# Optimization experiments

Measured on AMD Instinct MI355X. Metric: run time of the kernel, lower is better.

## Reference

```python
import jax, jax.numpy as jnp
import numpy as np

B, L, D = 2, 2048, 1024
H, HD = 16, 64
MAX_LEN = 4096


def rotate_half(t):
    t1, t2 = jnp.split(t, 2, axis=-1)
    return jnp.concatenate([-t2, t1], axis=-1)


def setup_inputs() -> dict:
    key = jax.random.key(0)
    ks = jax.random.split(key, 6)
    # rope tables computed the standard way (cos/sin of position*inv_freq)
    inv_freq = 1.0 / (10000.0 ** (np.arange(0, HD, 2, dtype=np.float32) / HD))
    pos = np.arange(MAX_LEN, dtype=np.float32)
    freqs = np.einsum('l,f->lf', pos, inv_freq)          # [MAX_LEN, HD/2]
    emb = np.concatenate([freqs, freqs], axis=-1)        # [MAX_LEN, HD]
    return {
        'x': jax.random.normal(ks[0], (B, L, D), dtype=jnp.float32),
        'rope_cos': jnp.asarray(np.cos(emb)),
        'rope_sin': jnp.asarray(np.sin(emb)),
        'W_qkv': jax.random.normal(ks[1], (D, 3 * H * HD), dtype=jnp.float32) * (D ** -0.5),
        'W_out': jax.random.normal(ks[2], (H * HD, D), dtype=jnp.float32) * ((H * HD) ** -0.5),
        'b_out': jnp.zeros((D,), dtype=jnp.float32),
    }


def reference(x, rope_cos, rope_sin, W_qkv, W_out, b_out):
    Bb, Ll, Dd = x.shape
    qkv = jnp.einsum('bld,de->ble', x, W_qkv)            # fused QKV projection
    q, k, v = jnp.split(qkv, 3, axis=-1)
    # [B, h, L, d]
    q = q.reshape(Bb, Ll, H, HD).transpose(0, 2, 1, 3)
    k = k.reshape(Bb, Ll, H, HD).transpose(0, 2, 1, 3)
    v = v.reshape(Bb, Ll, H, HD).transpose(0, 2, 1, 3)
    cos = rope_cos[:Ll][None, None, :, :]                # [1,1,L,d]
    sin = rope_sin[:Ll][None, None, :, :]
    q = q * cos + rotate_half(q) * sin
    k = k * cos + rotate_half(k) * sin
    # causal scaled dot-product attention
    scale = HD ** -0.5
    scores = jnp.einsum('bhqd,bhkd->bhqk', q, k) * scale
    causal = jnp.tril(jnp.ones((Ll, Ll), dtype=bool))
    scores = jnp.where(causal[None, None], scores, jnp.finfo(scores.dtype).min)
    attn = jax.nn.softmax(scores, axis=-1)
    out = jnp.einsum('bhqk,bhkd->bhqd', attn, v)
    out = out.transpose(0, 2, 1, 3).reshape(Bb, Ll, H * HD)
    return jnp.einsum('ble,ed->bld', out, W_out) + b_out
```

## Files before the change

kernel.cpp:

```cpp
#include <hip/hip_runtime.h>
#include <math.h>

#define BQ 2
#define LQ 2048
#define DQ 1024
#define HQ 16
#define HDQ 64

typedef __bf16 bf16_t;
typedef bf16_t bf16x4 __attribute__((ext_vector_type(4)));
typedef bf16_t bf16x8 __attribute__((ext_vector_type(8)));
typedef _Float16 f16_t;
typedef f16_t f16x4 __attribute__((ext_vector_type(4)));
typedef f16_t f16x8 __attribute__((ext_vector_type(8)));
typedef float f32x4 __attribute__((ext_vector_type(4)));

__global__ __launch_bounds__(256) void prep_kernel(
    const float* __restrict__ x, const float* __restrict__ Wqkv,
    const float* __restrict__ Wout, const float* __restrict__ cosT,
    const float* __restrict__ sinT,
    bf16_t* __restrict__ xb, bf16_t* __restrict__ Wqkvt,
    bf16_t* __restrict__ Wot, float4* __restrict__ rpk)
{
    __shared__ float t[32][33];
    const int bid = blockIdx.x, tid = threadIdx.x;
    if (bid < 4096) {
        const int i = (bid * 256 + tid) * 4;
        float4 v = *(const float4*)(x + i);
        bf16x4 o;
        o[0] = (bf16_t)v.x; o[1] = (bf16_t)v.y; o[2] = (bf16_t)v.z; o[3] = (bf16_t)v.w;
        *(bf16x4*)(xb + i) = o;
    } else if (bid < 8192) {
        const bool isq = bid < 7168;
        const int b = isq ? bid - 4096 : bid - 7168;
        const int N = isq ? 3072 : 1024;
        const int gx = isq ? 96 : 32;
        const float* in = isq ? Wqkv : Wout;
        bf16_t* out = isq ? Wqkvt : Wot;
        const int k0 = (b / gx) * 32, n0 = (b % gx) * 32;
        const int r = tid >> 3, c4 = (tid & 7) * 4;
        float4 v = *(const float4*)(in + (size_t)(k0 + r) * N + n0 + c4);
        t[r][c4 + 0] = v.x; t[r][c4 + 1] = v.y;
        t[r][c4 + 2] = v.z; t[r][c4 + 3] = v.w;
        __syncthreads();
        bf16x4 o;
        o[0] = (bf16_t)t[c4 + 0][r]; o[1] = (bf16_t)t[c4 + 1][r];
        o[2] = (bf16_t)t[c4 + 2][r]; o[3] = (bf16_t)t[c4 + 3][r];
        *(bf16x4*)(out + (size_t)(n0 + r) * 1024 + k0 + c4) = o;
    } else {
        const int idx = (bid - 8192) * 256 + tid;
        const int i = idx & 15, l = idx >> 4;
        rpk[idx] = make_float4(cosT[l * 64 + i], cosT[l * 64 + 16 + i],
                               sinT[l * 64 + i], sinT[l * 64 + 16 + i]);
    }
}

__global__ __launch_bounds__(256) void qkv_gemm_kernel(
    const bf16_t* __restrict__ A, const bf16_t* __restrict__ Bt,
    bf16_t* __restrict__ qo, bf16_t* __restrict__ ko, f16_t* __restrict__ vo,
    const float4* __restrict__ rpk)
{
    __shared__ __align__(16) bf16_t As[128][64];
    __shared__ __align__(16) bf16_t Bs[128][64];
    const int K = 1024;
    const int tid  = threadIdx.x;
    const int lane = tid & 63;
    const int w    = tid >> 6;
    const int lr   = lane & 15, quad = lane >> 4;
    const int wm   = w & 1, wn = w >> 1;
    const int m0   = blockIdx.y * 128, n0 = blockIdx.x * 128;
    const int srow8 = lane >> 3;
    const int swz   = ((lane & 7) ^ srow8) * 8;
    const int wc    = (lane & 7) * 8;

    f32x4 acc[4][4];
#pragma unroll
    for (int i = 0; i < 4; i++)
#pragma unroll
        for (int j = 0; j < 4; j++)
#pragma unroll
            for (int r = 0; r < 4; r++) acc[i][j][r] = 0.f;

    bf16x8 ar[4], br[4];
#pragma unroll
    for (int j = 0; j < 4; j++) {
        const int rr = (w * 4 + j) * 8 + srow8;
        ar[j] = *(const bf16x8*)(A  + (size_t)(m0 + rr) * K + swz);
        br[j] = *(const bf16x8*)(Bt + (size_t)(n0 + rr) * K + swz);
    }

    for (int k0 = 0; k0 < K; k0 += 64) {
        __syncthreads();
#pragma unroll
        for (int j = 0; j < 4; j++) {
            const int rg = (w * 4 + j) * 8 + srow8;
            *(bf16x8*)(&As[rg][wc]) = ar[j];
            *(bf16x8*)(&Bs[rg][wc]) = br[j];
        }
        __syncthreads();
        if (k0 + 64 < K) {
#pragma unroll
            for (int j = 0; j < 4; j++) {
                const int rr = (w * 4 + j) * 8 + srow8;
                ar[j] = *(const bf16x8*)(A  + (size_t)(m0 + rr) * K + k0 + 64 + swz);
                br[j] = *(const bf16x8*)(Bt + (size_t)(n0 + rr) * K + k0 + 64 + swz);
            }
        }

        bf16x8 af[4][2], bfr[4][2];
#pragma unroll
        for (int t = 0; t < 4; t++)
#pragma unroll
            for (int h = 0; h < 2; h++) {
                const int cA = ((quad + 4 * h) ^ (lr & 7)) * 8;
                af[t][h]  = *(const bf16x8*)(&As[wm * 64 + t * 16 + lr][cA]);
                bfr[t][h] = *(const bf16x8*)(&Bs[wn * 64 + t * 16 + lr][cA]);
            }
#pragma unroll
        for (int h = 0; h < 2; h++)
#pragma unroll
            for (int mt = 0; mt < 4; mt++)
#pragma unroll
                for (int nt = 0; nt < 4; nt++)
                    acc[mt][nt] = __builtin_amdgcn_mfma_f32_16x16x32_bf16(
                        af[mt][h], bfr[nt][h], acc[mt][nt], 0, 0, 0);
    }

    const int which = n0 >> 10;
    const int h = ((n0 & 1023) + wn * 64) >> 6;
    if (which == 2) {
#pragma unroll
        for (int mt = 0; mt < 4; mt++) {
            const int m = m0 + wm * 64 + mt * 16 + quad * 4;
            const int b = m >> 11, l = m & 2047;
            f16_t* p = vo + ((size_t)(b * HQ + h) * HDQ) * LQ + l;
#pragma unroll
            for (int nt = 0; nt < 4; nt++) {
                f16x4 pv;
#pragma unroll
                for (int r = 0; r < 4; r++) pv[r] = (f16_t)acc[mt][nt][r];
                *(f16x4*)(p + (size_t)(nt * 16 + lr) * LQ) = pv;
            }
        }
    } else {
        bf16_t* dst = which ? ko : qo;
        const float qs = which ? 1.0f : 0.18033688011f;
#pragma unroll
        for (int mt = 0; mt < 4; mt++)
#pragma unroll
            for (int r = 0; r < 4; r++) {
                const int m = m0 + wm * 64 + mt * 16 + quad * 4 + r;
                const int b = m >> 11, l = m & 2047;
                const float4 rp = rpk[l * 16 + lr];
                const float a0 = acc[mt][0][r], a1 = acc[mt][1][r];
                const float a2 = acc[mt][2][r], a3 = acc[mt][3][r];
                bf16_t* p = dst + ((size_t)(b * HQ + h) * LQ + l) * HDQ;
                p[lr]      = (bf16_t)((a0 * rp.x - a2 * rp.z) * qs);
                p[16 + lr] = (bf16_t)((a1 * rp.y - a3 * rp.w) * qs);
                p[32 + lr] = (bf16_t)((a2 * rp.x + a0 * rp.z) * qs);
                p[48 + lr] = (bf16_t)((a3 * rp.y + a1 * rp.w) * qs);
            }
    }
}

__global__ __launch_bounds__(256) void out_gemm_kernel(
    const bf16_t* __restrict__ A, const bf16_t* __restrict__ Bt,
    float* __restrict__ fo, const float* __restrict__ bias)
{
    __shared__ __align__(16) bf16_t As[64][64];
    __shared__ __align__(16) bf16_t Bs[128][64];
    const int K = 1024, N = 1024;
    const int tid  = threadIdx.x;
    const int lane = tid & 63;
    const int w    = tid >> 6;
    const int lr   = lane & 15, quad = lane >> 4;
    const int m0   = blockIdx.y * 64, n0 = blockIdx.x * 128;
    const int srow8 = lane >> 3;
    const int swz   = ((lane & 7) ^ srow8) * 8;
    const int wc    = (lane & 7) * 8;

    f32x4 acc[4][2];
#pragma unroll
    for (int i = 0; i < 4; i++)
#pragma unroll
        for (int j = 0; j < 2; j++)
#pragma unroll
            for (int r = 0; r < 4; r++) acc[i][j][r] = 0.f;

    bf16x8 ar[2], br[4];
#pragma unroll
    for (int j = 0; j < 2; j++)
        ar[j] = *(const bf16x8*)(A + (size_t)(m0 + (w * 2 + j) * 8 + srow8) * K + swz);
#pragma unroll
    for (int j = 0; j < 4; j++)
        br[j] = *(const bf16x8*)(Bt + (size_t)(n0 + (w * 4 + j) * 8 + srow8) * K + swz);

    for (int k0 = 0; k0 < K; k0 += 64) {
        __syncthreads();
#pragma unroll
        for (int j = 0; j < 2; j++)
            *(bf16x8*)(&As[(w * 2 + j) * 8 + srow8][wc]) = ar[j];
#pragma unroll
        for (int j = 0; j < 4; j++)
            *(bf16x8*)(&Bs[(w * 4 + j) * 8 + srow8][wc]) = br[j];
        __syncthreads();
        if (k0 + 64 < K) {
#pragma unroll
            for (int j = 0; j < 2; j++)
                ar[j] = *(const bf16x8*)(A + (size_t)(m0 + (w * 2 + j) * 8 + srow8) * K
                                          + k0 + 64 + swz);
#pragma unroll
            for (int j = 0; j < 4; j++)
                br[j] = *(const bf16x8*)(Bt + (size_t)(n0 + (w * 4 + j) * 8 + srow8) * K
                                          + k0 + 64 + swz);
        }

        bf16x8 af[4][2], bfr[2][2];
#pragma unroll
        for (int h = 0; h < 2; h++) {
            const int cA = ((quad + 4 * h) ^ (lr & 7)) * 8;
#pragma unroll
            for (int t = 0; t < 4; t++)
                af[t][h] = *(const bf16x8*)(&As[t * 16 + lr][cA]);
#pragma unroll
            for (int t = 0; t < 2; t++)
                bfr[t][h] = *(const bf16x8*)(&Bs[w * 32 + t * 16 + lr][cA]);
        }
#pragma unroll
        for (int h = 0; h < 2; h++)
#pragma unroll
            for (int mt = 0; mt < 4; mt++)
#pragma unroll
                for (int nt = 0; nt < 2; nt++)
                    acc[mt][nt] = __builtin_amdgcn_mfma_f32_16x16x32_bf16(
                        af[mt][h], bfr[nt][h], acc[mt][nt], 0, 0, 0);
    }

#pragma unroll
    for (int nt = 0; nt < 2; nt++) {
        const int n = n0 + w * 32 + nt * 16 + lr;
        const float bj = bias[n];
#pragma unroll
        for (int mt = 0; mt < 4; mt++)
#pragma unroll
            for (int r = 0; r < 4; r++) {
                const int m = m0 + mt * 16 + quad * 4 + r;
                fo[(size_t)m * N + n] = acc[mt][nt][r] + bj;
            }
    }
}

__global__ __launch_bounds__(512) void attn_kernel10(
    const bf16_t* __restrict__ qb, const bf16_t* __restrict__ kb,
    const f16_t* __restrict__ vtb, bf16_t* __restrict__ ob)
{
    __shared__ __align__(16) bf16_t Kb[2][64][64];
    __shared__ __align__(16) f16_t  Vs[2][64][68];

    const int tid  = threadIdx.x;
    const int lane = tid & 63;
    const int w    = tid >> 6;
    const int quad = lane >> 4;
    const int lr   = lane & 15;
    const int bh   = blockIdx.x;
    const int qt2  = 15 - blockIdx.y;

    const bf16_t* Kh = kb  + (size_t)bh * LQ * HDQ;
    const f16_t*  Vh = vtb + (size_t)bh * HDQ * LQ;

    const int r0  = tid >> 3;
    const int c0  = (tid & 7) * 8;
    const int ksw = ((tid & 7) ^ (r0 & 7)) * 8;

    f16x4 ones;
#pragma unroll
    for (int j = 0; j < 4; j++) ones[j] = (f16_t)1.0f;

    const int qbase = qt2 * 128 + w * 16;
    const int qrow  = qbase + lr;
    const bf16_t* qp = qb + ((size_t)bh * LQ + qrow) * HDQ;
    const bf16x8 qa0 = *(const bf16x8*)(qp + quad * 8);
    const bf16x8 qa1 = *(const bf16x8*)(qp + 32 + quad * 8);

    const int nkt = 2 * qt2 + 2;

    bf16x8 kp = *(const bf16x8*)(Kh + (size_t)r0 * HDQ + c0);
    f16x8  vp = *(const f16x8*)(Vh + (size_t)r0 * LQ + c0);

    f32x4 Oacc[4], lacc;
#pragma unroll
    for (int d = 0; d < 4; d++)
#pragma unroll
        for (int r = 0; r < 4; r++) Oacc[d][r] = 0.f;
#pragma unroll
    for (int r = 0; r < 4; r++) lacc[r] = 0.f;

    for (int kt = 0; kt < nkt; kt++) {
        const int buf = kt & 1;
        *(bf16x8*)(&Kb[buf][r0][ksw]) = kp;
        *(f16x8*)(&Vs[buf][r0][c0]) = vp;
        __syncthreads();
        if (kt + 1 < nkt) {
            kp = *(const bf16x8*)(Kh + (size_t)((kt + 1) * 64 + r0) * HDQ + c0);
            vp = *(const f16x8*)(Vh + (size_t)r0 * LQ + (kt + 1) * 64 + c0);
        }

        if (kt * 64 <= qbase + 15) {
            f32x4 s[4];
            __builtin_amdgcn_s_setprio(1);
#pragma unroll
            for (int nt = 0; nt < 4; nt++) {
                const int rsw = lr & 7;
                const bf16x8 kf0 = *(const bf16x8*)(&Kb[buf][nt * 16 + lr][(quad ^ rsw) * 8]);
                const bf16x8 kf1 = *(const bf16x8*)(&Kb[buf][nt * 16 + lr][((quad + 4) ^ rsw) * 8]);
                f32x4 z = {0.f, 0.f, 0.f, 0.f};
                z = __builtin_amdgcn_mfma_f32_16x16x32_bf16(kf0, qa0, z, 0, 0, 0);
                z = __builtin_amdgcn_mfma_f32_16x16x32_bf16(kf1, qa1, z, 0, 0, 0);
                s[nt] = z;
            }
            __builtin_amdgcn_s_setprio(0);
            if (kt * 64 + 63 > qbase) {
#pragma unroll
                for (int nt = 0; nt < 4; nt++)
#pragma unroll
                    for (int r = 0; r < 4; r++)
                        if (kt * 64 + nt * 16 + quad * 4 + r > qrow) s[nt][r] = -INFINITY;
            }
            f16x4 pa[4];
#pragma unroll
            for (int nt = 0; nt < 4; nt++)
#pragma unroll
                for (int r = 0; r < 4; r++)
                    pa[nt][r] = (f16_t)__builtin_amdgcn_exp2f(s[nt][r]);

            __builtin_amdgcn_s_setprio(1);
#pragma unroll
            for (int d = 0; d < 4; d++)
#pragma unroll
                for (int nt = 0; nt < 4; nt++) {
                    const f16x4 vf = *(const f16x4*)(&Vs[buf][d * 16 + lr][nt * 16 + quad * 4]);
                    Oacc[d] = __builtin_amdgcn_mfma_f32_16x16x16f16(pa[nt], vf, Oacc[d], 0, 0, 0);
                }
#pragma unroll
            for (int nt = 0; nt < 4; nt++)
                lacc = __builtin_amdgcn_mfma_f32_16x16x16f16(pa[nt], ones, lacc, 0, 0, 0);
            __builtin_amdgcn_s_setprio(0);
        }
    }

    const int b = bh >> 4, h = bh & 15;
#pragma unroll
    for (int r = 0; r < 4; r++) {
        const float inv = 1.0f / lacc[r];
        const int q = qbase + quad * 4 + r;
        bf16_t* op = ob + ((size_t)(b * LQ + q)) * 1024 + h * 64;
#pragma unroll
        for (int d = 0; d < 4; d++)
            op[d * 16 + lr] = (bf16_t)(Oacc[d][r] * inv);
    }
}

extern "C" void kernel_launch(void* const* d_in, const int* in_sizes, int n_in,
                              void* d_out, int out_size, void* d_ws, size_t ws_size,
                              hipStream_t stream) {
    const float* x        = (const float*)d_in[0];
    const float* rope_cos = (const float*)d_in[1];
    const float* rope_sin = (const float*)d_in[2];
    const float* W_qkv    = (const float*)d_in[3];
    const float* W_out    = (const float*)d_in[4];
    const float* b_out    = (const float*)d_in[5];
    float* out = (float*)d_out;

    char* wsb = (char*)d_ws;
    bf16_t* xb    = (bf16_t*)(wsb);
    bf16_t* qbf   = (bf16_t*)(wsb + ((size_t)8  << 20));
    bf16_t* kbf   = (bf16_t*)(wsb + ((size_t)16 << 20));
    f16_t*  vth   = (f16_t*) (wsb + ((size_t)24 << 20));
    bf16_t* ob    = (bf16_t*)(wsb + ((size_t)32 << 20));
    bf16_t* Wqkvt = (bf16_t*)(wsb + ((size_t)40 << 20));
    bf16_t* Wot   = (bf16_t*)(wsb + ((size_t)46 << 20));
    float4* rpk   = (float4*)(wsb + ((size_t)48 << 20));

    prep_kernel<<<8320, 256, 0, stream>>>(x, W_qkv, W_out, rope_cos, rope_sin,
                                          xb, Wqkvt, Wot, rpk);

    dim3 g1(3072 / 128, 4096 / 128);
    qkv_gemm_kernel<<<g1, 256, 0, stream>>>(xb, Wqkvt, qbf, kbf, vth, rpk);

    dim3 g2(32, 16);
    attn_kernel10<<<g2, 512, 0, stream>>>(qbf, kbf, vth, ob);

    dim3 g3(1024 / 128, 4096 / 64);
    out_gemm_kernel<<<g3, 256, 0, stream>>>(ob, Wot, out, b_out);
}
```

Baseline: 172.3 us.

## Double-buffer QKV GEMM shared tiles with K=32 stages and two-deep register prefetch

Restructures the QKV projection GEMM main loop from single-buffered 64-wide K tiles to double-buffered 32-wide K tiles in LDS, with two register stages of global prefetch. Each iteration now has one barrier instead of two, so writes to one LDS buffer can overlap MFMA work on the other. The LDS swizzle is changed to match the narrower tiles. The trade-off is more loop iterations with fewer MFMAs per barrier, plus extra registers for the second prefetch stage.

```diff
diff --git a/kernel.cpp b/kernel.cpp
--- a/kernel.cpp
+++ b/kernel.cpp
@@ -60,8 +60,8 @@
     bf16_t* __restrict__ qo, bf16_t* __restrict__ ko, f16_t* __restrict__ vo,
     const float4* __restrict__ rpk)
 {
-    __shared__ __align__(16) bf16_t As[128][64];
-    __shared__ __align__(16) bf16_t Bs[128][64];
+    __shared__ __align__(16) bf16_t As[2][128][32];
+    __shared__ __align__(16) bf16_t Bs[2][128][32];
     const int K = 1024;
     const int tid  = threadIdx.x;
     const int lane = tid & 63;
@@ -69,9 +69,16 @@
     const int lr   = lane & 15, quad = lane >> 4;
     const int wm   = w & 1, wn = w >> 1;
     const int m0   = blockIdx.y * 128, n0 = blockIdx.x * 128;
-    const int srow8 = lane >> 3;
-    const int swz   = ((lane & 7) ^ srow8) * 8;
-    const int wc    = (lane & 7) * 8;
+
+    const int sr  = tid >> 2;
+    const int sc  = tid & 3;
+    const int sw  = (sc ^ ((sr >> 1) & 3)) * 8;
+    const int rdc = (quad ^ ((lr >> 1) & 3)) * 8;
+
+    const bf16_t* Ar0 = A  + (size_t)(m0 + sr) * K + sc * 8;
+    const bf16_t* Ar1 = A  + (size_t)(m0 + sr + 64) * K + sc * 8;
+    const bf16_t* Br0 = Bt + (size_t)(n0 + sr) * K + sc * 8;
+    const bf16_t* Br1 = Bt + (size_t)(n0 + sr + 64) * K + sc * 8;
 
     f32x4 acc[4][4];
 #pragma unroll
@@ -81,50 +88,53 @@
 #pragma unroll
             for (int r = 0; r < 4; r++) acc[i][j][r] = 0.f;
 
-    bf16x8 ar[4], br[4];
-#pragma unroll
-    for (int j = 0; j < 4; j++) {
-        const int rr = (w * 4 + j) * 8 + srow8;
-        ar[j] = *(const bf16x8*)(A  + (size_t)(m0 + rr) * K + swz);
-        br[j] = *(const bf16x8*)(Bt + (size_t)(n0 + rr) * K + swz);
-    }
-
-    for (int k0 = 0; k0 < K; k0 += 64) {
-        __syncthreads();
-#pragma unroll
-        for (int j = 0; j < 4; j++) {
-            const int rg = (w * 4 + j) * 8 + srow8;
-            *(bf16x8*)(&As[rg][wc]) = ar[j];
-            *(bf16x8*)(&Bs[rg][wc]) = br[j];
-        }
-        __syncthreads();
-        if (k0 + 64 < K) {
-#pragma unroll
-            for (int j = 0; j < 4; j++) {
-                const int rr = (w * 4 + j) * 8 + srow8;
-                ar[j] = *(const bf16x8*)(A  + (size_t)(m0 + rr) * K + k0 + 64 + swz);
-                br[j] = *(const bf16x8*)(Bt + (size_t)(n0 + rr) * K + k0 + 64 + swz);
-            }
-        }
-
-        bf16x8 af[4][2], bfr[4][2];
-#pragma unroll
-        for (int t = 0; t < 4; t++)
-#pragma unroll
-            for (int h = 0; h < 2; h++) {
-                const int cA = ((quad + 4 * h) ^ (lr & 7)) * 8;
-                af[t][h]  = *(const bf16x8*)(&As[wm * 64 + t * 16 + lr][cA]);
-                bfr[t][h] = *(const bf16x8*)(&Bs[wn * 64 + t * 16 + lr][cA]);
-            }
-#pragma unroll
-        for (int h = 0; h < 2; h++)
-#pragma unroll
-            for (int mt = 0; mt < 4; mt++)
-#pragma unroll
-                for (int nt = 0; nt < 4; nt++)
-                    acc[mt][nt] = __builtin_amdgcn_mfma_f32_16x16x32_bf16(
-                        af[mt][h], bfr[nt][h], acc[mt][nt], 0, 0, 0);
-    }
+#define QLOAD(A0, A1, B0, B1, t) do {                      \
+        A0 = *(const bf16x8*)(Ar0 + (t) * 32);             \
+        A1 = *(const bf16x8*)(Ar1 + (t) * 32);             \
+        B0 = *(const bf16x8*)(Br0 + (t) * 32);             \
+        B1 = *(const bf16x8*)(Br1 + (t) * 32);             \
+    } while (0)
+#define QWRITE(A0, A1, B0, B1, bf) do {                    \
+        *(bf16x8*)(&As[bf][sr][sw])      = A0;             \
+        *(bf16x8*)(&As[bf][sr + 64][sw]) = A1;             \
+        *(bf16x8*)(&Bs[bf][sr][sw])      = B0;             \
+        *(bf16x8*)(&Bs[bf][sr + 64][sw]) = B1;             \
+    } while (0)
+#define QCOMP(bf) do {                                                        \
+        bf16x8 af[4], bfr[4];                                                 \
+        _Pragma("unroll")                                                     \
+        for (int tt = 0; tt < 4; tt++) {                                      \
+            af[tt]  = *(const bf16x8*)(&As[bf][wm * 64 + tt * 16 + lr][rdc]); \
+            bfr[tt] = *(const bf16x8*)(&Bs[bf][wn * 64 + tt * 16 + lr][rdc]); \
+        }                                                                     \
+        _Pragma("unroll")                                                     \
+        for (int mt = 0; mt < 4; mt++)                                        \
+            _Pragma("unroll")                                                 \
+            for (int nt = 0; nt < 4; nt++)                                    \
+                acc[mt][nt] = __builtin_amdgcn_mfma_f32_16x16x32_bf16(        \
+                    af[mt], bfr[nt], acc[mt][nt], 0, 0, 0);                   \
+    } while (0)
+
+    bf16x8 a00, a10, b00, b10;
+    bf16x8 a01, a11, b01, b11;
+    QLOAD(a00, a10, b00, b10, 0);
+    QLOAD(a01, a11, b01, b11, 1);
+    QWRITE(a00, a10, b00, b10, 0);
+    __syncthreads();
+
+    for (int t = 0; t < 32; t += 2) {
+        if (t + 2 < 32) QLOAD(a00, a10, b00, b10, t + 2);
+        QCOMP(0);
+        QWRITE(a01, a11, b01, b11, 1);
+        __syncthreads();
+        if (t + 3 < 32) QLOAD(a01, a11, b01, b11, t + 3);
+        QCOMP(1);
+        if (t + 2 < 32) QWRITE(a00, a10, b00, b10, 0);
+        __syncthreads();
+    }
+#undef QLOAD
+#undef QWRITE
+#undef QCOMP
 
     const int which = n0 >> 10;
     const int h = ((n0 & 1023) + wn * 64) >> 6;
```

New measurement: 174.6 us. No clear change (+1.3%).
